# Optimization experiments

Hardware: AMD Instinct MI355X
Metric: run time of the kernel (lower is better)

## Reference

```python
import jax, jax.numpy as jnp
import numpy as np

N_HEADS = 16
N_KV_HEADS = 8
SOFTMAX_N = 1.0


def _apply_rope(t, cos, sin):
    # t: [B, S, H, HD]; cos/sin: [S, HD//2]
    tr = t[..., 0::2]
    ti = t[..., 1::2]
    c = cos[None, :, None, :]
    s = sin[None, :, None, :]
    out_r = tr * c - ti * s
    out_i = tr * s + ti * c
    # interleave back: (..., HD//2, 2) -> (..., HD)
    return jnp.stack([out_r, out_i], axis=-1).reshape(t.shape)


def setup_inputs() -> dict:
    key = jax.random.key(0)
    ks = jax.random.split(key, 7)
    B, S, D = 2, 2048, 2048
    HD = D // N_HEADS  # 128
    kv_dim = N_KV_HEADS * HD  # 1024
    # realistic RoPE frequencies
    theta = 10000.0
    inv_freq = 1.0 / (theta ** (np.arange(0, HD, 2, dtype=np.float32) / HD))
    angles = np.outer(np.arange(S, dtype=np.float32), inv_freq)  # [S, HD//2]
    scale = 0.02
    return {
        "x": jax.random.normal(ks[0], (B, S, D), dtype=jnp.float32),
        "freqs_cos": jnp.asarray(np.cos(angles), dtype=jnp.float32),
        "freqs_sin": jnp.asarray(np.sin(angles), dtype=jnp.float32),
        "wq": jax.random.normal(ks[1], (D, D), dtype=jnp.float32) * scale,
        "wk": jax.random.normal(ks[2], (D, kv_dim), dtype=jnp.float32) * scale,
        "wv": jax.random.normal(ks[3], (D, kv_dim), dtype=jnp.float32) * scale,
        "wo": jax.random.normal(ks[4], (D, D), dtype=jnp.float32) * scale,
    }


def reference(x, freqs_cos, freqs_sin, wq, wk, wv, wo):
    B, S, D = x.shape
    HD = D // N_HEADS
    n_rep = N_HEADS // N_KV_HEADS

    xq = (x @ wq).reshape(B, S, N_HEADS, HD)
    xk = (x @ wk).reshape(B, S, N_KV_HEADS, HD)
    xv = (x @ wv).reshape(B, S, N_KV_HEADS, HD)

    xq = _apply_rope(xq, freqs_cos, freqs_sin)
    xk = _apply_rope(xk, freqs_cos, freqs_sin)

    # repeat_kv == repeat_interleave along head dim
    xk = jnp.repeat(xk, n_rep, axis=2)
    xv = jnp.repeat(xv, n_rep, axis=2)

    q = xq.transpose(0, 2, 1, 3)  # [B,H,S,HD]
    k = xk.transpose(0, 2, 1, 3)
    v = xv.transpose(0, 2, 1, 3)

    scores = jnp.einsum('bhqd,bhkd->bhqk', q, k) / jnp.sqrt(jnp.float32(HD))
    causal = jnp.tril(jnp.ones((S, S), dtype=bool))
    scores = jnp.where(causal[None, None], scores, -jnp.inf)

    # softmax-n with shifted-zeros correction (NOT shift symmetric)
    m = jnp.max(scores, axis=-1, keepdims=True)
    e = jnp.exp(scores - m)
    denom = jnp.sum(e, axis=-1, keepdims=True) + SOFTMAX_N * jnp.exp(-m)
    attn = e / denom

    out = jnp.einsum('bhqk,bhkd->bhqd', attn, v)
    out = out.transpose(0, 2, 1, 3).reshape(B, S, D)
    return out @ wo
```

## Files before the change

### kernel.cpp

```cpp
#include <hip/hip_runtime.h>

typedef unsigned short u16;
typedef u16 u16x8 __attribute__((ext_vector_type(8)));
typedef u16 u16x4 __attribute__((ext_vector_type(4)));
typedef __bf16 bf16x8 __attribute__((ext_vector_type(8)));
typedef float f32x4 __attribute__((ext_vector_type(4)));

__device__ __forceinline__ u16 f2bf(float x) {
  unsigned u = __builtin_bit_cast(unsigned, x);
  u = (u + 0x7FFFu + ((u >> 16) & 1u)) >> 16;
  return (u16)u;
}

#define GLOAD16(gp, lp)                                                        \
  __builtin_amdgcn_global_load_lds(                                            \
      (const __attribute__((address_space(1))) unsigned int*)(gp),             \
      (__attribute__((address_space(3))) unsigned int*)(lp), 16, 0, 0)

__global__ __launch_bounds__(256) void k_cvt(const float* __restrict__ in, u16* __restrict__ out, int n4) {
  int i = blockIdx.x * 256 + threadIdx.x;
  if (i >= n4) return;
  float4 v = ((const float4*)in)[i];
  u16x4 o;
  o[0] = f2bf(v.x); o[1] = f2bf(v.y); o[2] = f2bf(v.z); o[3] = f2bf(v.w);
  ((u16x4*)out)[i] = o;
}

__global__ __launch_bounds__(256) void k_cvt_t(const float* __restrict__ in, u16* __restrict__ out, int R, int C) {
  __shared__ u16 t[64][72];
  int c0 = blockIdx.x * 64, r0 = blockIdx.y * 64;
  int tid = threadIdx.x;
  int rl = tid >> 2;
  int cl0 = (tid & 3) * 16;
#pragma unroll
  for (int j = 0; j < 4; ++j) {
    float4 v = *(const float4*)&in[(size_t)(r0 + rl) * C + c0 + cl0 + j * 4];
    t[rl][cl0 + j * 4 + 0] = f2bf(v.x);
    t[rl][cl0 + j * 4 + 1] = f2bf(v.y);
    t[rl][cl0 + j * 4 + 2] = f2bf(v.z);
    t[rl][cl0 + j * 4 + 3] = f2bf(v.w);
  }
  __syncthreads();
  int cr = tid >> 2;
  int s0 = (tid & 3) * 16;
  __align__(16) u16 tmp[16];
#pragma unroll
  for (int k = 0; k < 16; ++k) tmp[k] = t[s0 + k][cr];
  *(u16x8*)&out[(size_t)(c0 + cr) * R + r0 + s0]     = *(u16x8*)&tmp[0];
  *(u16x8*)&out[(size_t)(c0 + cr) * R + r0 + s0 + 8] = *(u16x8*)&tmp[8];
}

template <bool F32OUT>
__global__ __launch_bounds__(256) void k_gemm(const u16* __restrict__ A, const u16* __restrict__ Bt,
                                              void* __restrict__ Cout, int M, int N, int K) {
  __shared__ __align__(16) u16 lA[128 * 64];
  __shared__ __align__(16) u16 lB[128 * 64];
  int m0 = blockIdx.x * 128, n0 = blockIdx.y * 128;
  int tid = threadIdx.x;
  int wid = tid >> 6, lane = tid & 63;
  int fr = lane & 15, fg = lane >> 4;
  int wm = (wid & 1) * 64, wn = (wid >> 1) * 64;
  int srow = tid >> 3, scu = (tid & 7) * 8;
  f32x4 acc[4][4] = {};
  const int nk = K >> 6;
  for (int kt = 0; kt < nk; ++kt) {
    int k0 = kt << 6;
#pragma unroll
    for (int r = 0; r < 4; ++r) {
      int row = srow + r * 32;
      int swz = scu ^ ((row & 7) << 3);
      GLOAD16(&A[(size_t)(m0 + row) * K + k0 + swz],  &lA[row * 64 + scu]);
      GLOAD16(&Bt[(size_t)(n0 + row) * K + k0 + swz], &lB[row * 64 + scu]);
    }
    __syncthreads();
#pragma unroll
    for (int kh = 0; kh < 2; ++kh) {
      bf16x8 af[4], bf[4];
#pragma unroll
      for (int mi = 0; mi < 4; ++mi) {
        int row = wm + mi * 16 + fr;
        af[mi] = *(const bf16x8*)&lA[row * 64 + ((kh * 32 + fg * 8) ^ ((row & 7) << 3))];
      }
#pragma unroll
      for (int ni = 0; ni < 4; ++ni) {
        int row = wn + ni * 16 + fr;
        bf[ni] = *(const bf16x8*)&lB[row * 64 + ((kh * 32 + fg * 8) ^ ((row & 7) << 3))];
      }
#pragma unroll
      for (int mi = 0; mi < 4; ++mi)
#pragma unroll
        for (int ni = 0; ni < 4; ++ni)
          acc[mi][ni] = __builtin_amdgcn_mfma_f32_16x16x32_bf16(af[mi], bf[ni], acc[mi][ni], 0, 0, 0);
    }
    __syncthreads();
  }
#pragma unroll
  for (int mi = 0; mi < 4; ++mi)
#pragma unroll
    for (int ni = 0; ni < 4; ++ni)
#pragma unroll
      for (int r = 0; r < 4; ++r) {
        int row = m0 + wm + mi * 16 + fg * 4 + r;
        int col = n0 + wn + ni * 16 + fr;
        float v = acc[mi][ni][r];
        if (F32OUT) ((float*)Cout)[(size_t)row * N + col] = v;
        else        ((u16*)Cout)[(size_t)row * N + col] = f2bf(v);
      }
}

__global__ __launch_bounds__(256) void k_rope(const u16* __restrict__ qkv, const float* __restrict__ fc,
                                              const float* __restrict__ fs, u16* __restrict__ Qr,
                                              u16* __restrict__ Kr) {
  int row = blockIdx.x;
  int b = row >> 11, s = row & 2047;
  int tid = threadIdx.x;
  float4 c4 = *(const float4*)&fc[s * 64 + (tid & 15) * 4];
  float4 s4 = *(const float4*)&fs[s * 64 + (tid & 15) * 4];
  float cc[4] = {c4.x, c4.y, c4.z, c4.w};
  float ss[4] = {s4.x, s4.y, s4.z, s4.w};
  {
    bf16x8 v = *(const bf16x8*)&qkv[(size_t)row * 4096 + tid * 8];
    bf16x8 o;
    const float qs = 0.08838834764831845f;
#pragma unroll
    for (int j = 0; j < 4; ++j) {
      float e = (float)v[2 * j], od = (float)v[2 * j + 1];
      o[2 * j]     = (__bf16)((e * cc[j] - od * ss[j]) * qs);
      o[2 * j + 1] = (__bf16)((e * ss[j] + od * cc[j]) * qs);
    }
    int h = tid >> 4, d0 = (tid & 15) * 8;
    *(bf16x8*)&Qr[(((size_t)(b * 16 + h)) * 2048 + s) * 128 + d0] = o;
  }
  if (tid < 128) {
    bf16x8 v = *(const bf16x8*)&qkv[(size_t)row * 4096 + 2048 + tid * 8];
    bf16x8 o;
#pragma unroll
    for (int j = 0; j < 4; ++j) {
      float e = (float)v[2 * j], od = (float)v[2 * j + 1];
      o[2 * j]     = (__bf16)(e * cc[j] - od * ss[j]);
      o[2 * j + 1] = (__bf16)(e * ss[j] + od * cc[j]);
    }
    int hk = tid >> 4, d0 = (tid & 15) * 8;
    *(bf16x8*)&Kr[(((size_t)(b * 8 + hk)) * 2048 + s) * 128 + d0] = o;
  }
}

__global__ __launch_bounds__(256) void k_vtrans(const u16* __restrict__ qkv, u16* __restrict__ Vt) {
  __shared__ u16 t[64][72];
  int dt = blockIdx.x, st = blockIdx.y, bh = blockIdx.z;
  int b = bh >> 3, hk = bh & 7;
  int s0 = st * 64, d0 = dt * 64;
  int tid = threadIdx.x;
  int rl = tid >> 3, cs = (tid & 7) * 8;
#pragma unroll
  for (int rnd = 0; rnd < 2; ++rnd) {
    int srow = rl + rnd * 32;
    u16x8 v = *(const u16x8*)&qkv[(size_t)(b * 2048 + s0 + srow) * 4096 + 3072 + hk * 128 + d0 + cs];
#pragma unroll
    for (int k = 0; k < 8; ++k) t[srow][cs + k] = v[k];
  }
  __syncthreads();
#pragma unroll
  for (int rnd = 0; rnd < 2; ++rnd) {
    int drow = rl + rnd * 32;
    u16x8 o;
#pragma unroll
    for (int k = 0; k < 8; ++k) o[k] = t[cs + k][drow];
    *(u16x8*)&Vt[((size_t)(b * 8 + hk) * 128 + d0 + drow) * 2048 + s0 + cs] = o;
  }
}

__global__ __launch_bounds__(256) void k_attn(const u16* __restrict__ Qr, const u16* __restrict__ Kr,
                                              const u16* __restrict__ Vt, u16* __restrict__ Og) {
  const int S = 2048;
  __shared__ __align__(16) u16 lK[2][64 * 128];
  __shared__ __align__(16) u16 lV[2][128 * 64];
  __shared__ __align__(16) u16 lP[4][16 * 64];
  int h = blockIdx.y, b = blockIdx.z;
  int hk = h >> 1;
  int tid = threadIdx.x, wid = tid >> 6, lane = tid & 63;
  int fr = lane & 15, fg = lane >> 4;
  const size_t kvbase = ((size_t)(b * 8 + hk)) * S * 128;
  int ksr = tid >> 4, ksc = (tid & 15) * 8;
  int vsr = tid >> 3, vsc = (tid & 7) * 8;
  int kswz = ksc ^ ((ksr & 7) << 3);
  int vswz = vsc ^ ((vsr & 7) << 3);

#define STAGE_KV(K0, BUF)                                                                      \
  {                                                                                            \
    int k0_ = (K0);                                                                            \
    _Pragma("unroll")                                                                          \
    for (int r = 0; r < 4; ++r) {                                                              \
      GLOAD16(&Kr[kvbase + (size_t)(k0_ + ksr + r * 16) * 128 + kswz],                         \
              &lK[BUF][(ksr + r * 16) * 128 + ksc]);                                           \
      GLOAD16(&Vt[kvbase + (size_t)(vsr + r * 32) * S + k0_ + vswz],                           \
              &lV[BUF][(vsr + r * 32) * 64 + vsc]);                                            \
    }                                                                                          \
  }

  for (int pp = 0; pp < 2; ++pp) {
    int qt = pp == 0 ? (31 - (int)blockIdx.x) : (int)blockIdx.x;
    int q0 = qt * 64;
    int qw = q0 + wid * 16;
    bf16x8 qf[4];
    {
      const u16* qb = Qr + (((size_t)(b * 16 + h)) * S + qw) * 128;
#pragma unroll
      for (int ds = 0; ds < 4; ++ds)
        qf[ds] = *(const bf16x8*)&qb[fr * 128 + ds * 32 + fg * 8];
    }
    f32x4 acc[8] = {};
    float mR[4] = {-1e30f, -1e30f, -1e30f, -1e30f};
    float lR[4] = {0.f, 0.f, 0.f, 0.f};
    int nt = qt + 1;
    STAGE_KV(0, 0);
    __syncthreads();
    int cur = 0;
    for (int t = 0; t < nt; ++t) {
      int k0 = t * 64;
      if (t + 1 < nt) STAGE_KV(k0 + 64, cur ^ 1);
      f32x4 sf[4] = {};
#pragma unroll
      for (int kb = 0; kb < 4; ++kb)
#pragma unroll
        for (int ds = 0; ds < 4; ++ds) {
          int row = kb * 16 + fr;
          bf16x8 kf = *(const bf16x8*)&lK[cur][row * 128 + ((ds * 32 + fg * 8) ^ ((row & 7) << 3))];
          sf[kb] = __builtin_amdgcn_mfma_f32_16x16x32_bf16(qf[ds], kf, sf[kb], 0, 0, 0);
        }
      if (k0 + 63 > qw) {
#pragma unroll
        for (int kb = 0; kb < 4; ++kb)
#pragma unroll
          for (int r = 0; r < 4; ++r)
            if (k0 + kb * 16 + fr > qw + fg * 4 + r) sf[kb][r] = -1e30f;
      }
      float mnew[4], scl[4];
#pragma unroll
      for (int r = 0; r < 4; ++r) {
        float v = fmaxf(fmaxf(sf[0][r], sf[1][r]), fmaxf(sf[2][r], sf[3][r]));
        v = fmaxf(v, __shfl_xor(v, 1));
        v = fmaxf(v, __shfl_xor(v, 2));
        v = fmaxf(v, __shfl_xor(v, 4));
        v = fmaxf(v, __shfl_xor(v, 8));
        mnew[r] = fmaxf(mR[r], v);
        scl[r] = __expf(mR[r] - mnew[r]);
        mR[r] = mnew[r];
      }
#pragma unroll
      for (int kb = 0; kb < 4; ++kb)
#pragma unroll
        for (int r = 0; r < 4; ++r)
          sf[kb][r] = __expf(sf[kb][r] - mnew[r]);
#pragma unroll
      for (int r = 0; r < 4; ++r) {
        float sum = sf[0][r] + sf[1][r] + sf[2][r] + sf[3][r];
        sum += __shfl_xor(sum, 1);
        sum += __shfl_xor(sum, 2);
        sum += __shfl_xor(sum, 4);
        sum += __shfl_xor(sum, 8);
        lR[r] = lR[r] * scl[r] + sum;
      }
#pragma unroll
      for (int kb = 0; kb < 4; ++kb)
#pragma unroll
        for (int r = 0; r < 4; ++r) {
          int q = fg * 4 + r;
          int cu = kb * 16 + fr;
          lP[wid][q * 64 + (cu ^ ((q & 7) << 3))] = f2bf(sf[kb][r]);
        }
#pragma unroll
      for (int ni = 0; ni < 8; ++ni)
#pragma unroll
        for (int r = 0; r < 4; ++r)
          acc[ni][r] *= scl[r];
#pragma unroll
      for (int kh = 0; kh < 2; ++kh) {
        bf16x8 pf = *(const bf16x8*)&lP[wid][fr * 64 + ((kh * 32 + fg * 8) ^ ((fr & 7) << 3))];
#pragma unroll
        for (int ni = 0; ni < 8; ++ni) {
          int row = ni * 16 + fr;
          bf16x8 vf = *(const bf16x8*)&lV[cur][row * 64 + ((kh * 32 + fg * 8) ^ ((row & 7) << 3))];
          acc[ni] = __builtin_amdgcn_mfma_f32_16x16x32_bf16(pf, vf, acc[ni], 0, 0, 0);
        }
      }
      __syncthreads();
      cur ^= 1;
    }
    float rden[4];
#pragma unroll
    for (int r = 0; r < 4; ++r) rden[r] = 1.0f / (lR[r] + __expf(-mR[r]));
#pragma unroll
    for (int ni = 0; ni < 8; ++ni)
#pragma unroll
      for (int r = 0; r < 4; ++r) {
        int q = qw + fg * 4 + r;
        int col = h * 128 + ni * 16 + fr;
        Og[((size_t)(b * S + q)) * 2048 + col] = f2bf(acc[ni][r] * rden[r]);
      }
  }
#undef STAGE_KV
}

extern "C" void kernel_launch(void* const* d_in, const int* in_sizes, int n_in,
                              void* d_out, int out_size, void* d_ws, size_t ws_size,
                              hipStream_t stream) {
  const float* x  = (const float*)d_in[0];
  const float* fc = (const float*)d_in[1];
  const float* fs = (const float*)d_in[2];
  const float* wq = (const float*)d_in[3];
  const float* wk = (const float*)d_in[4];
  const float* wv = (const float*)d_in[5];
  const float* wo = (const float*)d_in[6];

  char* p = (char*)d_ws;
  u16* xb    = (u16*)p; p += (size_t)4096 * 2048 * 2;
  u16* wqkvt = (u16*)p; p += (size_t)4096 * 2048 * 2;
  u16* wot   = (u16*)p; p += (size_t)2048 * 2048 * 2;
  u16* qkv   = (u16*)p; p += (size_t)4096 * 4096 * 2;
  u16* Qr    = (u16*)p; p += (size_t)2 * 16 * 2048 * 128 * 2;
  u16* Kr    = (u16*)p; p += (size_t)2 * 8 * 2048 * 128 * 2;
  u16* Vt    = (u16*)p; p += (size_t)2 * 8 * 2048 * 128 * 2;
  u16* Og    = xb;

  k_cvt<<<8192, 256, 0, stream>>>(x, xb, 2097152);
  k_cvt_t<<<dim3(32, 32), 256, 0, stream>>>(wq, wqkvt, 2048, 2048);
  k_cvt_t<<<dim3(16, 32), 256, 0, stream>>>(wk, wqkvt + (size_t)2048 * 2048, 2048, 1024);
  k_cvt_t<<<dim3(16, 32), 256, 0, stream>>>(wv, wqkvt + (size_t)3072 * 2048, 2048, 1024);
  k_cvt_t<<<dim3(32, 32), 256, 0, stream>>>(wo, wot, 2048, 2048);
  k_gemm<false><<<dim3(32, 32), 256, 0, stream>>>(xb, wqkvt, qkv, 4096, 4096, 2048);
  k_rope<<<4096, 256, 0, stream>>>(qkv, fc, fs, Qr, Kr);
  k_vtrans<<<dim3(2, 32, 16), 256, 0, stream>>>(qkv, Vt);
  k_attn<<<dim3(16, 16, 2), 256, 0, stream>>>(Qr, Kr, Vt, Og);
  k_gemm<true><<<dim3(32, 16), 256, 0, stream>>>(Og, wot, d_out, 4096, 2048, 2048);
}
```

Before: 375.0 us.

## Use lazy max rescaling, deferred row-sum reduction, and MFMA priority hints in attention

Rewrites the online softmax so the running max and the accumulator are rescaled only when some wave's new row max exceeds the old one by more than 8, which skips per-tile exp and multiply work on most iterations. The row-sum cross-lane shuffle reduction moves out of the loop and runs once at the end. The bf16 conversion switches to a native cast, and s_setprio wraps the MFMA sections to favour matrix issue across waves. The deferred max means exponentials can reach up to e^8 before rescaling, which relies on fp32 and bf16 headroom. The exp(-m) correction term still uses the stored max, which stays consistent with the lazily updated accumulator.

```diff
diff --git a/kernel.cpp b/kernel.cpp
--- a/kernel.cpp
+++ b/kernel.cpp
@@ -211,7 +211,7 @@
     }
     f32x4 acc[8] = {};
     float mR[4] = {-1e30f, -1e30f, -1e30f, -1e30f};
-    float lR[4] = {0.f, 0.f, 0.f, 0.f};
+    float lRp[4] = {0.f, 0.f, 0.f, 0.f};
     int nt = qt + 1;
     STAGE_KV(0, 0);
     __syncthreads();
@@ -220,6 +220,7 @@
       int k0 = t * 64;
       if (t + 1 < nt) STAGE_KV(k0 + 64, cur ^ 1);
       f32x4 sf[4] = {};
+      __builtin_amdgcn_s_setprio(1);
 #pragma unroll
       for (int kb = 0; kb < 4; ++kb)
 #pragma unroll
@@ -228,6 +229,7 @@
           bf16x8 kf = *(const bf16x8*)&lK[cur][row * 128 + ((ds * 32 + fg * 8) ^ ((row & 7) << 3))];
           sf[kb] = __builtin_amdgcn_mfma_f32_16x16x32_bf16(qf[ds], kf, sf[kb], 0, 0, 0);
         }
+      __builtin_amdgcn_s_setprio(0);
       if (k0 + 63 > qw) {
 #pragma unroll
         for (int kb = 0; kb < 4; ++kb)
@@ -235,7 +237,7 @@
           for (int r = 0; r < 4; ++r)
             if (k0 + kb * 16 + fr > qw + fg * 4 + r) sf[kb][r] = -1e30f;
       }
-      float mnew[4], scl[4];
+      float pm[4];
 #pragma unroll
       for (int r = 0; r < 4; ++r) {
         float v = fmaxf(fmaxf(sf[0][r], sf[1][r]), fmaxf(sf[2][r], sf[3][r]));
@@ -243,37 +245,38 @@
         v = fmaxf(v, __shfl_xor(v, 2));
         v = fmaxf(v, __shfl_xor(v, 4));
         v = fmaxf(v, __shfl_xor(v, 8));
-        mnew[r] = fmaxf(mR[r], v);
-        scl[r] = __expf(mR[r] - mnew[r]);
-        mR[r] = mnew[r];
+        pm[r] = v;
+      }
+      bool grow = (pm[0] > mR[0] + 8.f) | (pm[1] > mR[1] + 8.f) |
+                  (pm[2] > mR[2] + 8.f) | (pm[3] > mR[3] + 8.f);
+      if (__any(grow)) {
+#pragma unroll
+        for (int r = 0; r < 4; ++r) {
+          float mn = fmaxf(mR[r], pm[r]);
+          float sc = __expf(mR[r] - mn);
+          mR[r] = mn;
+          lRp[r] *= sc;
+#pragma unroll
+          for (int ni = 0; ni < 8; ++ni) acc[ni][r] *= sc;
+        }
       }
 #pragma unroll
       for (int kb = 0; kb < 4; ++kb)
 #pragma unroll
         for (int r = 0; r < 4; ++r)
-          sf[kb][r] = __expf(sf[kb][r] - mnew[r]);
-#pragma unroll
-      for (int r = 0; r < 4; ++r) {
-        float sum = sf[0][r] + sf[1][r] + sf[2][r] + sf[3][r];
-        sum += __shfl_xor(sum, 1);
-        sum += __shfl_xor(sum, 2);
-        sum += __shfl_xor(sum, 4);
-        sum += __shfl_xor(sum, 8);
-        lR[r] = lR[r] * scl[r] + sum;
-      }
+          sf[kb][r] = __expf(sf[kb][r] - mR[r]);
+#pragma unroll
+      for (int r = 0; r < 4; ++r)
+        lRp[r] += (sf[0][r] + sf[1][r]) + (sf[2][r] + sf[3][r]);
 #pragma unroll
       for (int kb = 0; kb < 4; ++kb)
 #pragma unroll
         for (int r = 0; r < 4; ++r) {
           int q = fg * 4 + r;
           int cu = kb * 16 + fr;
-          lP[wid][q * 64 + (cu ^ ((q & 7) << 3))] = f2bf(sf[kb][r]);
+          lP[wid][q * 64 + (cu ^ ((q & 7) << 3))] = __builtin_bit_cast(u16, (__bf16)sf[kb][r]);
         }
-#pragma unroll
-      for (int ni = 0; ni < 8; ++ni)
-#pragma unroll
-        for (int r = 0; r < 4; ++r)
-          acc[ni][r] *= scl[r];
+      __builtin_amdgcn_s_setprio(1);
 #pragma unroll
       for (int kh = 0; kh < 2; ++kh) {
         bf16x8 pf = *(const bf16x8*)&lP[wid][fr * 64 + ((kh * 32 + fg * 8) ^ ((fr & 7) << 3))];
@@ -284,12 +287,20 @@
           acc[ni] = __builtin_amdgcn_mfma_f32_16x16x32_bf16(pf, vf, acc[ni], 0, 0, 0);
         }
       }
+      __builtin_amdgcn_s_setprio(0);
       __syncthreads();
       cur ^= 1;
     }
     float rden[4];
 #pragma unroll
-    for (int r = 0; r < 4; ++r) rden[r] = 1.0f / (lR[r] + __expf(-mR[r]));
+    for (int r = 0; r < 4; ++r) {
+      float s = lRp[r];
+      s += __shfl_xor(s, 1);
+      s += __shfl_xor(s, 2);
+      s += __shfl_xor(s, 4);
+      s += __shfl_xor(s, 8);
+      rden[r] = 1.0f / (s + __expf(-mR[r]));
+    }
 #pragma unroll
     for (int ni = 0; ni < 8; ++ni)
 #pragma unroll
```

After: 360.9 us. 1.04x faster.

## Transpose QK^T MFMA, lazy max rescale, register-shuffled P instead of LDS

Applied to the files above, without the earlier changes.

Swaps the MFMA operands so each lane holds scores for a single query row, which reduces the row max and sum to two cross-group shuffles and one scalar per lane. The running max is only updated, and the accumulator rescaled, when the new block max exceeds it by more than 8, which skips most rescale work. The P tile is packed to bf16 in registers and redistributed with lane shuffles instead of a round trip through LDS, and s_setprio is raised around the MFMA sections. The lazy threshold keeps results exact in principle, because the stale max still appears in the final exp(-m) term, but it lets values grow up to e^8 before rescaling. The shuffle-based P layout adds many ds_bpermute operations.

```diff
diff --git a/kernel.cpp b/kernel.cpp
--- a/kernel.cpp
+++ b/kernel.cpp
@@ -3,6 +3,7 @@
 typedef unsigned short u16;
 typedef u16 u16x8 __attribute__((ext_vector_type(8)));
 typedef u16 u16x4 __attribute__((ext_vector_type(4)));
+typedef unsigned u32x4 __attribute__((ext_vector_type(4)));
 typedef __bf16 bf16x8 __attribute__((ext_vector_type(8)));
 typedef float f32x4 __attribute__((ext_vector_type(4)));
 
@@ -175,7 +176,6 @@
   const int S = 2048;
   __shared__ __align__(16) u16 lK[2][64 * 128];
   __shared__ __align__(16) u16 lV[2][128 * 64];
-  __shared__ __align__(16) u16 lP[4][16 * 64];
   int h = blockIdx.y, b = blockIdx.z;
   int hk = h >> 1;
   int tid = threadIdx.x, wid = tid >> 6, lane = tid & 63;
@@ -210,8 +210,8 @@
         qf[ds] = *(const bf16x8*)&qb[fr * 128 + ds * 32 + fg * 8];
     }
     f32x4 acc[8] = {};
-    float mR[4] = {-1e30f, -1e30f, -1e30f, -1e30f};
-    float lR[4] = {0.f, 0.f, 0.f, 0.f};
+    float mR = -1e30f;
+    float lRp = 0.f;
     int nt = qt + 1;
     STAGE_KV(0, 0);
     __syncthreads();
@@ -220,63 +220,75 @@
       int k0 = t * 64;
       if (t + 1 < nt) STAGE_KV(k0 + 64, cur ^ 1);
       f32x4 sf[4] = {};
+      __builtin_amdgcn_s_setprio(1);
 #pragma unroll
       for (int kb = 0; kb < 4; ++kb)
 #pragma unroll
         for (int ds = 0; ds < 4; ++ds) {
           int row = kb * 16 + fr;
           bf16x8 kf = *(const bf16x8*)&lK[cur][row * 128 + ((ds * 32 + fg * 8) ^ ((row & 7) << 3))];
-          sf[kb] = __builtin_amdgcn_mfma_f32_16x16x32_bf16(qf[ds], kf, sf[kb], 0, 0, 0);
+          sf[kb] = __builtin_amdgcn_mfma_f32_16x16x32_bf16(kf, qf[ds], sf[kb], 0, 0, 0);
         }
+      __builtin_amdgcn_s_setprio(0);
       if (k0 + 63 > qw) {
 #pragma unroll
         for (int kb = 0; kb < 4; ++kb)
 #pragma unroll
           for (int r = 0; r < 4; ++r)
-            if (k0 + kb * 16 + fr > qw + fg * 4 + r) sf[kb][r] = -1e30f;
-      }
-      float mnew[4], scl[4];
-#pragma unroll
-      for (int r = 0; r < 4; ++r) {
-        float v = fmaxf(fmaxf(sf[0][r], sf[1][r]), fmaxf(sf[2][r], sf[3][r]));
-        v = fmaxf(v, __shfl_xor(v, 1));
-        v = fmaxf(v, __shfl_xor(v, 2));
-        v = fmaxf(v, __shfl_xor(v, 4));
-        v = fmaxf(v, __shfl_xor(v, 8));
-        mnew[r] = fmaxf(mR[r], v);
-        scl[r] = __expf(mR[r] - mnew[r]);
-        mR[r] = mnew[r];
+            if (k0 + kb * 16 + fg * 4 + r > qw + fr) sf[kb][r] = -1e30f;
+      }
+      float pm;
+      {
+        float v0 = fmaxf(fmaxf(sf[0][0], sf[0][1]), fmaxf(sf[0][2], sf[0][3]));
+        float v1 = fmaxf(fmaxf(sf[1][0], sf[1][1]), fmaxf(sf[1][2], sf[1][3]));
+        float v2 = fmaxf(fmaxf(sf[2][0], sf[2][1]), fmaxf(sf[2][2], sf[2][3]));
+        float v3 = fmaxf(fmaxf(sf[3][0], sf[3][1]), fmaxf(sf[3][2], sf[3][3]));
+        pm = fmaxf(fmaxf(v0, v1), fmaxf(v2, v3));
+        pm = fmaxf(pm, __shfl_xor(pm, 16));
+        pm = fmaxf(pm, __shfl_xor(pm, 32));
+      }
+      if (__any(pm > mR + 8.f)) {
+        float mn = fmaxf(mR, pm);
+        float sc = __expf(mR - mn);
+        mR = mn;
+        lRp *= sc;
+        float sc4[4];
+#pragma unroll
+        for (int r = 0; r < 4; ++r) sc4[r] = __shfl(sc, fg * 4 + r);
+#pragma unroll
+        for (int ni = 0; ni < 8; ++ni)
+#pragma unroll
+          for (int r = 0; r < 4; ++r) acc[ni][r] *= sc4[r];
       }
 #pragma unroll
       for (int kb = 0; kb < 4; ++kb)
 #pragma unroll
         for (int r = 0; r < 4; ++r)
-          sf[kb][r] = __expf(sf[kb][r] - mnew[r]);
-#pragma unroll
-      for (int r = 0; r < 4; ++r) {
-        float sum = sf[0][r] + sf[1][r] + sf[2][r] + sf[3][r];
-        sum += __shfl_xor(sum, 1);
-        sum += __shfl_xor(sum, 2);
-        sum += __shfl_xor(sum, 4);
-        sum += __shfl_xor(sum, 8);
-        lR[r] = lR[r] * scl[r] + sum;
-      }
+          sf[kb][r] = __expf(sf[kb][r] - mR);
+      lRp += ((sf[0][0] + sf[0][1] + sf[0][2] + sf[0][3]) + (sf[1][0] + sf[1][1] + sf[1][2] + sf[1][3]))
+           + ((sf[2][0] + sf[2][1] + sf[2][2] + sf[2][3]) + (sf[3][0] + sf[3][1] + sf[3][2] + sf[3][3]));
+      unsigned pk[4][2];
 #pragma unroll
       for (int kb = 0; kb < 4; ++kb)
 #pragma unroll
-        for (int r = 0; r < 4; ++r) {
-          int q = fg * 4 + r;
-          int cu = kb * 16 + fr;
-          lP[wid][q * 64 + (cu ^ ((q & 7) << 3))] = f2bf(sf[kb][r]);
+        for (int hh = 0; hh < 2; ++hh) {
+          unsigned lo = (unsigned)__builtin_bit_cast(u16, (__bf16)sf[kb][2 * hh]);
+          unsigned hi = (unsigned)__builtin_bit_cast(u16, (__bf16)sf[kb][2 * hh + 1]);
+          pk[kb][hh] = lo | (hi << 16);
         }
-#pragma unroll
-      for (int ni = 0; ni < 8; ++ni)
-#pragma unroll
-        for (int r = 0; r < 4; ++r)
-          acc[ni][r] *= scl[r];
+      __builtin_amdgcn_s_setprio(1);
 #pragma unroll
       for (int kh = 0; kh < 2; ++kh) {
-        bf16x8 pf = *(const bf16x8*)&lP[wid][fr * 64 + ((kh * 32 + fg * 8) ^ ((fr & 7) << 3))];
+        unsigned dw[4];
+#pragma unroll
+        for (int d = 0; d < 4; ++d) {
+          int src = ((2 * (fg & 1) + (d >> 1)) << 4) + fr;
+          unsigned a = (unsigned)__shfl((int)pk[2 * kh][d & 1], src);
+          unsigned bsel = (unsigned)__shfl((int)pk[2 * kh + 1][d & 1], src);
+          dw[d] = (fg & 2) ? bsel : a;
+        }
+        u32x4 dwv = {dw[0], dw[1], dw[2], dw[3]};
+        bf16x8 pf = __builtin_bit_cast(bf16x8, dwv);
 #pragma unroll
         for (int ni = 0; ni < 8; ++ni) {
           int row = ni * 16 + fr;
@@ -284,19 +296,24 @@
           acc[ni] = __builtin_amdgcn_mfma_f32_16x16x32_bf16(pf, vf, acc[ni], 0, 0, 0);
         }
       }
+      __builtin_amdgcn_s_setprio(0);
       __syncthreads();
       cur ^= 1;
     }
-    float rden[4];
-#pragma unroll
-    for (int r = 0; r < 4; ++r) rden[r] = 1.0f / (lR[r] + __expf(-mR[r]));
+    float s = lRp;
+    s += __shfl_xor(s, 16);
+    s += __shfl_xor(s, 32);
+    float rden = 1.0f / (s + __expf(-mR));
+    float rd4[4];
+#pragma unroll
+    for (int r = 0; r < 4; ++r) rd4[r] = __shfl(rden, fg * 4 + r);
 #pragma unroll
     for (int ni = 0; ni < 8; ++ni)
 #pragma unroll
       for (int r = 0; r < 4; ++r) {
         int q = qw + fg * 4 + r;
         int col = h * 128 + ni * 16 + fr;
-        Og[((size_t)(b * S + q)) * 2048 + col] = f2bf(acc[ni][r] * rden[r]);
+        Og[((size_t)(b * S + q)) * 2048 + col] = f2bf(acc[ni][r] * rd4[r]);
       }
   }
 #undef STAGE_KV
```

Measured after the change: 355.5 us. 5.2% less time.
